# Kernel tuning notes

Hardware: AMD Instinct MI355X
Metric: run time of the kernel (lower is better)

## Reference

```python
import jax, jax.numpy as jnp
import numpy as np

B, N, D = 2, 2048, 1024          # batch, seq (= wh*ww), model dim
H, HD = 16, 64                   # heads, head_dim (inner_dim = H*HD = D)
MLP = 4096                       # SwiGLU hidden dim
WSY, WSX = 16, 32                # ws_y = wh//2, ws_x = ww//2  (wh=32, ww=64)
EPS = float(jnp.finfo(jnp.float32).eps)  # torch RMSNorm default eps


def setup_inputs() -> dict:
    key = jax.random.key(0)
    ks = jax.random.split(key, 8)
    return {
        "x": jax.random.normal(ks[0], (B, N, D), jnp.float32),
        "t": jax.random.normal(ks[1], (B,), jnp.float32),
        "dt": jax.random.normal(ks[2], (B, D), jnp.float32),
        "w_qkv": (jax.random.normal(ks[3], (3 * H * HD, D), jnp.float32) * 0.02),
        "w_o": (jax.random.normal(ks[4], (D, H * HD), jnp.float32) * 0.02),
        "w1": (jax.random.normal(ks[5], (2 * MLP, D), jnp.float32) * 0.02),
        "w2": (jax.random.normal(ks[6], (D, MLP), jnp.float32) * 0.02),
        "g_attn": jnp.ones((D,), jnp.float32),  # RMSNorm weight (attn)
        "g_ff": jnp.ones((D,), jnp.float32),    # RMSNorm weight (ffn)
    }


def _rms(x, g):
    return x * jax.lax.rsqrt(jnp.mean(x * x, axis=-1, keepdims=True) + EPS) * g


def _win(x):
    # 'b h (wc_y wc_x ws_y ws_x) d' -> 'b h (wc_y ws_y wc_x ws_x) d'
    b, h, n, d = x.shape
    return x.reshape(b, h, 2, 2, WSY, WSX, d).transpose(0, 1, 2, 4, 3, 5, 6).reshape(b, h, n, d)


def _unwin(x):
    # inverse of _win
    b, h, n, d = x.shape
    return x.reshape(b, h, 2, WSY, 2, WSX, d).transpose(0, 1, 2, 4, 3, 5, 6).reshape(b, h, n, d)


def reference(x, t, dt, w_qkv, w_o, w1, w2, g_attn, g_ff):
    # ---- SPAttention (pre-norm); all-to-all is identity on 1 device ----
    h = _rms(x, g_attn)
    qkv = h @ w_qkv.T                              # [B,N,3*H*HD]
    q, k, v = jnp.split(qkv, 3, axis=-1)
    as_heads = lambda z: z.reshape(B, N, H, HD).transpose(0, 2, 1, 3)  # b h n d
    q, k, v = _win(as_heads(q)), _win(as_heads(k)), _win(as_heads(v))
    # NOTE: the source computes RoPE2D(q), RoPE2D(k) but discards the result;
    # attention consumes the UNROTATED seq_gathered_q/k/v. Faithful: no rotation.
    scale = 1.0 / jnp.sqrt(jnp.float32(HD))        # SDPA default scale
    s = jnp.einsum('bhqd,bhkd->bhqk', q, k) * scale
    a = jax.nn.softmax(s, axis=-1)
    o = jnp.einsum('bhqk,bhkd->bhqd', a, v)
    o = _unwin(o).transpose(0, 2, 1, 3).reshape(B, N, H * HD)
    x = x + o @ w_o.T                               # residual
    # ---- SwiGLU FeedForward (pre-norm) + residual ----
    hf = _rms(x, g_ff)
    gate, up = jnp.split(hf @ w1.T, 2, axis=-1)
    return x + (jax.nn.silu(gate) * up) @ w2.T
```

## Files before the change

### kernel.cpp

```cpp
#include <hip/hip_runtime.h>
#include <cstdint>
#include <cstddef>

typedef __attribute__((ext_vector_type(8)))  __bf16 bf16x8;
typedef __attribute__((ext_vector_type(4)))  __bf16 bf16x4;
typedef __attribute__((ext_vector_type(4)))  float  f32x4;
typedef __attribute__((ext_vector_type(16))) float  f32x16;
typedef __attribute__((ext_vector_type(2)))  uint32_t u32x2;
typedef __attribute__((ext_vector_type(4)))  uint32_t u32x4;

#define MFMA_BF16(a, b, c) __builtin_amdgcn_mfma_f32_16x16x32_bf16((a), (b), (c), 0, 0, 0)
#define MFMA32(a, b, c)    __builtin_amdgcn_mfma_f32_32x32x16_bf16((a), (b), (c), 0, 0, 0)

__device__ __forceinline__ void gload_lds16(const __bf16* src, __bf16* lds_dst) {
    __builtin_amdgcn_global_load_lds(
        (const __attribute__((address_space(1))) void*)(const_cast<__bf16*>(src)),
        (__attribute__((address_space(3))) void*)(lds_dst), 16, 0, 0);
}

__device__ __forceinline__ uint32_t pack2(float a, float b) {
    uint16_t ua = __builtin_bit_cast(uint16_t, (__bf16)a);
    uint16_t ub = __builtin_bit_cast(uint16_t, (__bf16)b);
    return (uint32_t)ua | ((uint32_t)ub << 16);
}

__device__ __forceinline__ int xcd_swz(int lid, int n) {
    return (lid & 7) * (n >> 3) + (lid >> 3);
}

__global__ __launch_bounds__(256) void cvt4_kernel(const float* __restrict__ s0,
                                                   const float* __restrict__ s1,
                                                   const float* __restrict__ s2,
                                                   const float* __restrict__ s3,
                                                   __bf16* __restrict__ d0,
                                                   __bf16* __restrict__ d1,
                                                   __bf16* __restrict__ d2,
                                                   __bf16* __restrict__ d3) {
    int b = blockIdx.x;
    const float* s; __bf16* d; int off;
    if (b < 3072)       { s = s0; d = d0; off = b; }
    else if (b < 4096)  { s = s1; d = d1; off = b - 3072; }
    else if (b < 12288) { s = s2; d = d2; off = b - 4096; }
    else                { s = s3; d = d3; off = b - 12288; }
    int i = off * 256 + threadIdx.x;
    float4 v = reinterpret_cast<const float4*>(s)[i];
    bf16x4 o;
    o[0] = (__bf16)v.x; o[1] = (__bf16)v.y; o[2] = (__bf16)v.z; o[3] = (__bf16)v.w;
    reinterpret_cast<bf16x4*>(d)[i] = o;
}

__global__ __launch_bounds__(256) void rmsnorm_kernel(const float* __restrict__ x,
                                                      const float* __restrict__ g,
                                                      __bf16* __restrict__ out) {
    const int row = blockIdx.x;
    const int t = threadIdx.x;
    float4 v = reinterpret_cast<const float4*>(x + (size_t)row * 1024)[t];
    float ss = v.x * v.x + v.y * v.y + v.z * v.z + v.w * v.w;
#pragma unroll
    for (int m = 1; m < 64; m <<= 1) ss += __shfl_xor(ss, m);
    __shared__ float sred[4];
    if ((t & 63) == 0) sred[t >> 6] = ss;
    __syncthreads();
    float tot = sred[0] + sred[1] + sred[2] + sred[3];
    float rs = rsqrtf(tot * (1.0f / 1024.0f) + 1.1920928955078125e-07f);
    float4 gv = reinterpret_cast<const float4*>(g)[t];
    bf16x4 o;
    o[0] = (__bf16)(v.x * rs * gv.x);
    o[1] = (__bf16)(v.y * rs * gv.y);
    o[2] = (__bf16)(v.z * rs * gv.z);
    o[3] = (__bf16)(v.w * rs * gv.w);
    *reinterpret_cast<bf16x4*>(out + (size_t)row * 1024 + t * 4) = o;
}

__global__ __launch_bounds__(256) void rmsnorm_b_kernel(const __bf16* __restrict__ x,
                                                        const float* __restrict__ g,
                                                        __bf16* __restrict__ out) {
    const int row = blockIdx.x;
    const int t = threadIdx.x;
    bf16x4 v4 = reinterpret_cast<const bf16x4*>(x + (size_t)row * 1024)[t];
    float a = (float)v4[0], b = (float)v4[1], c = (float)v4[2], d = (float)v4[3];
    float ss = a * a + b * b + c * c + d * d;
#pragma unroll
    for (int m = 1; m < 64; m <<= 1) ss += __shfl_xor(ss, m);
    __shared__ float sred[4];
    if ((t & 63) == 0) sred[t >> 6] = ss;
    __syncthreads();
    float tot = sred[0] + sred[1] + sred[2] + sred[3];
    float rs = rsqrtf(tot * (1.0f / 1024.0f) + 1.1920928955078125e-07f);
    float4 gv = reinterpret_cast<const float4*>(g)[t];
    bf16x4 o;
    o[0] = (__bf16)(a * rs * gv.x);
    o[1] = (__bf16)(b * rs * gv.y);
    o[2] = (__bf16)(c * rs * gv.z);
    o[3] = (__bf16)(d * rs * gv.w);
    *reinterpret_cast<bf16x4*>(out + (size_t)row * 1024 + t * 4) = o;
}

template <int MODE, int NB>
__global__ __launch_bounds__(256) void gemm_nt(const __bf16* __restrict__ A, int lda,
                                               const __bf16* __restrict__ B, int ldb,
                                               __bf16* __restrict__ outb,
                                               float* __restrict__ outf,
                                               const float* __restrict__ resid,
                                               const __bf16* __restrict__ residb,
                                               int K, int ldo) {
    constexpr int BN = NB * 32;
    __shared__ __attribute__((aligned(16))) __bf16 As[128 * 64];
    __shared__ __attribute__((aligned(16))) __bf16 Bs[BN * 64];
    const int t = threadIdx.x;
    const int lane = t & 63;
    const int wid = t >> 6;
    const int nwg = gridDim.x * gridDim.y;
    const int sid = xcd_swz(blockIdx.x + blockIdx.y * gridDim.x, nwg);
    const int bm = sid % gridDim.x, bn = sid / gridDim.x;
    const int wm = (wid >> 1) * 64, wn = (wid & 1) * (NB * 16);
    f32x4 acc[4][NB] = {};

    for (int kt = 0; kt < K; kt += 64) {
        __syncthreads();
#pragma unroll
        for (int i = 0; i < 4; ++i) {
            int L = i * 256 + t;
            int r = L >> 3, s = L & 7;
            int c = s ^ (r & 7);
            gload_lds16(A + (size_t)(bm * 128 + r) * lda + kt + c * 8, As + L * 8);
        }
#pragma unroll
        for (int i = 0; i < NB; ++i) {
            int L = i * 256 + t;
            int r = L >> 3, s = L & 7;
            int c = s ^ (r & 7);
            int rb = bn * BN + r;
            int srow = (MODE == 2) ? ((rb >> 1) + ((rb & 1) << 12)) : rb;
            gload_lds16(B + (size_t)srow * ldb + kt + c * 8, Bs + L * 8);
        }
        __syncthreads();
#pragma unroll
        for (int ks = 0; ks < 2; ++ks) {
            bf16x8 af[4], bfr[NB];
#pragma unroll
            for (int mi = 0; mi < 4; ++mi) {
                int r = wm + mi * 16 + (lane & 15);
                int slot = (ks * 4 + (lane >> 4)) ^ (r & 7);
                af[mi] = *reinterpret_cast<const bf16x8*>(As + r * 64 + slot * 8);
            }
#pragma unroll
            for (int ni = 0; ni < NB; ++ni) {
                int r = wn + ni * 16 + (lane & 15);
                int slot = (ks * 4 + (lane >> 4)) ^ (r & 7);
                bfr[ni] = *reinterpret_cast<const bf16x8*>(Bs + r * 64 + slot * 8);
            }
            __builtin_amdgcn_s_setprio(1);
#pragma unroll
            for (int mi = 0; mi < 4; ++mi)
#pragma unroll
                for (int ni = 0; ni < NB; ++ni)
                    acc[mi][ni] = MFMA_BF16(af[mi], bfr[ni], acc[mi][ni]);
            __builtin_amdgcn_s_setprio(0);
        }
    }
    const int row0 = bm * 128 + wm + ((lane >> 4) << 2);
    const int col0 = bn * BN + wn + (lane & 15);
#pragma unroll
    for (int mi = 0; mi < 4; ++mi)
#pragma unroll
        for (int ni = 0; ni < NB; ++ni)
#pragma unroll
            for (int r2 = 0; r2 < 4; ++r2) {
                int row = row0 + mi * 16 + r2;
                int col = col0 + ni * 16;
                float v = acc[mi][ni][r2];
                size_t idx = (size_t)row * ldo + col;
                if (MODE == 0) {
                    outb[idx] = (__bf16)v;
                } else if (MODE == 1) {
                    outb[idx] = (__bf16)(v + resid[idx]);
                } else if (MODE == 3) {
                    outf[idx] = v + (float)residb[idx];
                } else {
                    float pv = __shfl_xor(v, 1);
                    if (!(lane & 1)) {
                        float sg = v / (1.0f + __expf(-v));
                        outb[(size_t)row * ldo + (col >> 1)] = (__bf16)(sg * pv);
                    }
                }
            }
}

__global__ __launch_bounds__(256) void vtrans_kernel(const __bf16* __restrict__ qkv,
                                                     __bf16* __restrict__ vt) {
    __shared__ __bf16 T[64][68];
    const int t = threadIdx.x;
    const int bh = blockIdx.y, b = bh >> 4, h = bh & 15;
    const int n0 = blockIdx.x * 64;
    const __bf16* vp = qkv + (size_t)b * 2048 * 3072 + 2048 + h * 64;
#pragma unroll
    for (int i = 0; i < 2; ++i) {
        int r = i * 32 + (t >> 3), c = t & 7;
        bf16x8 v = *reinterpret_cast<const bf16x8*>(vp + (size_t)(n0 + r) * 3072 + c * 8);
#pragma unroll
        for (int j = 0; j < 8; ++j) T[c * 8 + j][r] = v[j];
    }
    __syncthreads();
#pragma unroll
    for (int i = 0; i < 2; ++i) {
        int hd = i * 32 + (t >> 3), c = t & 7;
        bf16x8 v;
#pragma unroll
        for (int j = 0; j < 8; ++j) v[j] = T[hd][c * 8 + j];
        *reinterpret_cast<bf16x8*>(vt + ((size_t)bh * 64 + hd) * 2048 + n0 + c * 8) = v;
    }
}

__global__ __launch_bounds__(256) void attn_kernel(const __bf16* __restrict__ qkv,
                                                   const __bf16* __restrict__ vt,
                                                   __bf16* __restrict__ o) {
    __shared__ __attribute__((aligned(16))) __bf16 Ks[2][128 * 64];
    __shared__ __attribute__((aligned(16))) __bf16 Vs[2][64 * 128];
    const int t = threadIdx.x;
    const int lane = t & 63;
    const int w = t >> 6;
    const int hi = lane >> 5;
    const int l31 = lane & 31;
    const int nwg = gridDim.x * gridDim.y;
    const int sid = xcd_swz(blockIdx.x + blockIdx.y * gridDim.x, nwg);
    const int qb = sid % gridDim.x;
    const int bh = sid / gridDim.x;
    const int b = bh >> 4, h = bh & 15;
    const __bf16* qp = qkv + (size_t)b * 2048 * 3072 + h * 64;
    const __bf16* kp = qp + 1024;
    const __bf16* vtp = vt + (size_t)bh * 64 * 2048;
    const int q0 = qb * 128 + w * 32;

    const float SC = 0.18033688011112042f;
    bf16x8 qf[4];
#pragma unroll
    for (int s = 0; s < 4; ++s) {
        bf16x8 raw = *reinterpret_cast<const bf16x8*>(
            qp + (size_t)(q0 + l31) * 3072 + s * 16 + hi * 8);
        bf16x8 sc;
#pragma unroll
        for (int j = 0; j < 8; ++j) sc[j] = (__bf16)((float)raw[j] * SC);
        qf[s] = sc;
    }

    f32x16 oa[2] = {};
    float l_run = 0.0f;

    auto stage = [&](int buf, int kt) {
#pragma unroll
        for (int i = 0; i < 4; ++i) {
            int L = i * 256 + t;
            int r = L >> 3, s = L & 7;
            int c = s ^ (r & 7);
            gload_lds16(kp + (size_t)(kt + r) * 3072 + c * 8, &Ks[buf][L * 8]);
        }
#pragma unroll
        for (int i = 0; i < 4; ++i) {
            int L = i * 256 + t;
            int r = L >> 4, s = L & 15;
            int c = s ^ (r & 15);
            gload_lds16(vtp + (size_t)r * 2048 + kt + c * 8, &Vs[buf][L * 8]);
        }
    };
    stage(0, 0);
    __syncthreads();

    for (int kt = 0; kt < 2048; kt += 128) {
        const int buf = (kt >> 7) & 1;
        if (kt + 128 < 2048) stage(buf ^ 1, kt + 128);

#pragma unroll
        for (int h2 = 0; h2 < 2; ++h2) {
            f32x16 st[2];
#pragma unroll
            for (int r = 0; r < 16; ++r) { st[0][r] = -6.0f; st[1][r] = -6.0f; }
            __builtin_amdgcn_s_setprio(1);
#pragma unroll
            for (int s = 0; s < 4; ++s) {
#pragma unroll
                for (int mb = 0; mb < 2; ++mb) {
                    int r = h2 * 64 + mb * 32 + l31;
                    int sl = (s * 2 + hi) ^ (r & 7);
                    bf16x8 kf = *reinterpret_cast<const bf16x8*>(&Ks[buf][r * 64 + sl * 8]);
                    st[mb] = MFMA32(kf, qf[s], st[mb]);
                }
            }
            __builtin_amdgcn_s_setprio(0);

            float ps = 0.0f;
#pragma unroll
            for (int mb = 0; mb < 2; ++mb)
#pragma unroll
                for (int r = 0; r < 16; ++r) {
                    float p = exp2f(st[mb][r]);
                    st[mb][r] = p;
                    ps += p;
                }
            ps += __shfl_xor(ps, 32);
            l_run += ps;

            uint32_t pk[16];
#pragma unroll
            for (int mb = 0; mb < 2; ++mb)
#pragma unroll
                for (int i2 = 0; i2 < 8; ++i2)
                    pk[mb * 8 + i2] = pack2(st[mb][2 * i2], st[mb][2 * i2 + 1]);

            __builtin_amdgcn_s_setprio(1);
#pragma unroll
            for (int s2 = 0; s2 < 4; ++s2) {
                const int I0 = (s2 >> 1) * 8 + (s2 & 1) * 4;
                u32x2 w02 = __builtin_amdgcn_permlane32_swap(pk[I0], pk[I0 + 2], false, false);
                u32x2 w13 = __builtin_amdgcn_permlane32_swap(pk[I0 + 1], pk[I0 + 3], false, false);
                u32x4 fv;
                fv[0] = w02[0]; fv[1] = w13[0]; fv[2] = w02[1]; fv[3] = w13[1];
                bf16x8 pa = __builtin_bit_cast(bf16x8, fv);
#pragma unroll
                for (int nb = 0; nb < 2; ++nb) {
                    int rv = nb * 32 + l31;
                    int ch = h2 * 8 + s2 * 2 + hi;
                    int sl = ch ^ (rv & 15);
                    bf16x8 vf = *reinterpret_cast<const bf16x8*>(&Vs[buf][rv * 128 + sl * 8]);
                    oa[nb] = MFMA32(pa, vf, oa[nb]);
                }
            }
            __builtin_amdgcn_s_setprio(0);
        }
        __syncthreads();
    }

#pragma unroll
    for (int r = 0; r < 16; ++r) {
        int crow = (r & 3) + 8 * (r >> 2) + 4 * hi;
        float lv = __shfl(l_run, crow);
        float inv = 1.0f / lv;
        int row = q0 + crow;
        size_t base = ((size_t)b * 2048 + row) * 1024 + h * 64 + l31;
        o[base]      = (__bf16)(oa[0][r] * inv);
        o[base + 32] = (__bf16)(oa[1][r] * inv);
    }
}

extern "C" void kernel_launch(void* const* d_in, const int* in_sizes, int n_in,
                              void* d_out, int out_size, void* d_ws, size_t ws_size,
                              hipStream_t stream) {
    const float* x      = (const float*)d_in[0];
    const float* w_qkv  = (const float*)d_in[3];
    const float* w_o    = (const float*)d_in[4];
    const float* w1     = (const float*)d_in[5];
    const float* w2     = (const float*)d_in[6];
    const float* g_attn = (const float*)d_in[7];
    const float* g_ff   = (const float*)d_in[8];
    float* out = (float*)d_out;

    char* ws = (char*)d_ws;
    size_t off = 0;
    auto alloc = [&](size_t bytes) -> void* {
        void* p = ws + off;
        off += (bytes + 255) & ~(size_t)255;
        return p;
    };
    __bf16* wqkv_b = (__bf16*)alloc((size_t)3072 * 1024 * 2);
    __bf16* wo_b   = (__bf16*)alloc((size_t)1024 * 1024 * 2);
    __bf16* w1_b   = (__bf16*)alloc((size_t)8192 * 1024 * 2);
    __bf16* w2_b   = (__bf16*)alloc((size_t)1024 * 4096 * 2);
    __bf16* h_b    = (__bf16*)alloc((size_t)4096 * 1024 * 2);
    __bf16* qkv_b  = (__bf16*)alloc((size_t)4096 * 3072 * 2);
    __bf16* o_b    = (__bf16*)alloc((size_t)4096 * 1024 * 2);
    __bf16* x2b    = (__bf16*)alloc((size_t)4096 * 1024 * 2);
    __bf16* vt_b   = (__bf16*)alloc((size_t)32 * 64 * 2048 * 2);
    __bf16* act_b  = qkv_b;

    cvt4_kernel<<<16384, 256, 0, stream>>>(w_qkv, w_o, w1, w2,
                                           wqkv_b, wo_b, w1_b, w2_b);

    rmsnorm_kernel<<<4096, 256, 0, stream>>>(x, g_attn, h_b);
    gemm_nt<0, 4><<<dim3(32, 24), 256, 0, stream>>>(h_b, 1024, wqkv_b, 1024,
                                                    qkv_b, nullptr, nullptr, nullptr,
                                                    1024, 3072);
    vtrans_kernel<<<dim3(32, 32), 256, 0, stream>>>(qkv_b, vt_b);
    attn_kernel<<<dim3(16, 32), 256, 0, stream>>>(qkv_b, vt_b, o_b);
    gemm_nt<1, 2><<<dim3(32, 16), 256, 0, stream>>>(o_b, 1024, wo_b, 1024,
                                                    x2b, nullptr, x, nullptr,
                                                    1024, 1024);
    rmsnorm_b_kernel<<<4096, 256, 0, stream>>>(x2b, g_ff, h_b);
    gemm_nt<2, 4><<<dim3(32, 64), 256, 0, stream>>>(h_b, 1024, w1_b, 1024,
                                                    act_b, nullptr, nullptr, nullptr,
                                                    1024, 4096);
    gemm_nt<3, 4><<<dim3(32, 8), 256, 0, stream>>>(act_b, 4096, w2_b, 4096,
                                                   nullptr, out, nullptr, x2b,
                                                   4096, 1024);
}
```

Baseline: 317.0 us.

## Split-K attention, fuse V transpose into QKV GEMM, retile FFN GEMMs

The QKV GEMM epilogue now writes the V part directly in transposed layout, which removes the separate transpose kernel. Attention is split into two key halves along a grid z dimension. Each half writes unnormalized fp32 partial outputs and row sums, and a new combine kernel merges them. The attention loop also drops LDS double buffering in favor of load-then-barrier. The w1 GEMM gets a square-ish block-swizzle mapping, and the w2 GEMM uses NB=2 with twice as many blocks. These changes add parallelism and remove a kernel, but they add fp32 partial traffic and lose the load/compute overlap in attention.

```diff
diff --git a/kernel.cpp b/kernel.cpp
--- a/kernel.cpp
+++ b/kernel.cpp
@@ -96,13 +96,14 @@
     *reinterpret_cast<bf16x4*>(out + (size_t)row * 1024 + t * 4) = o;
 }
 
-template <int MODE, int NB>
+template <int MODE, int NB, int SQ>
 __global__ __launch_bounds__(256) void gemm_nt(const __bf16* __restrict__ A, int lda,
                                                const __bf16* __restrict__ B, int ldb,
                                                __bf16* __restrict__ outb,
                                                float* __restrict__ outf,
                                                const float* __restrict__ resid,
                                                const __bf16* __restrict__ residb,
+                                               __bf16* __restrict__ vt,
                                                int K, int ldo) {
     constexpr int BN = NB * 32;
     __shared__ __attribute__((aligned(16))) __bf16 As[128 * 64];
@@ -110,9 +111,17 @@
     const int t = threadIdx.x;
     const int lane = t & 63;
     const int wid = t >> 6;
-    const int nwg = gridDim.x * gridDim.y;
-    const int sid = xcd_swz(blockIdx.x + blockIdx.y * gridDim.x, nwg);
-    const int bm = sid % gridDim.x, bn = sid / gridDim.x;
+    int bm, bn;
+    if (SQ) {
+        int lid = blockIdx.x + blockIdx.y * gridDim.x;
+        int c = lid & 7, i = lid >> 3;
+        bm = (c & 1) * 16 + (i & 15);
+        bn = (c >> 1) * 16 + (i >> 4);
+    } else {
+        int nwg = gridDim.x * gridDim.y;
+        int sid = xcd_swz(blockIdx.x + blockIdx.y * gridDim.x, nwg);
+        bm = sid % gridDim.x; bn = sid / gridDim.x;
+    }
     const int wm = (wid >> 1) * 64, wn = (wid & 1) * (NB * 16);
     f32x4 acc[4][NB] = {};
 
@@ -161,6 +170,22 @@
     }
     const int row0 = bm * 128 + wm + ((lane >> 4) << 2);
     const int col0 = bn * BN + wn + (lane & 15);
+    if (MODE == 4 && bn >= 16) {
+#pragma unroll
+        for (int mi = 0; mi < 4; ++mi)
+#pragma unroll
+            for (int ni = 0; ni < NB; ++ni) {
+                bf16x4 o4;
+#pragma unroll
+                for (int r2 = 0; r2 < 4; ++r2) o4[r2] = (__bf16)acc[mi][ni][r2];
+                int n0 = row0 + mi * 16;
+                int bb = n0 >> 11, nn = n0 & 2047;
+                int vc = col0 + ni * 16 - 2048;
+                *reinterpret_cast<bf16x4*>(
+                    vt + ((size_t)(bb * 16 + (vc >> 6)) * 64 + (vc & 63)) * 2048 + nn) = o4;
+            }
+        return;
+    }
 #pragma unroll
     for (int mi = 0; mi < 4; ++mi)
 #pragma unroll
@@ -171,7 +196,7 @@
                 int col = col0 + ni * 16;
                 float v = acc[mi][ni][r2];
                 size_t idx = (size_t)row * ldo + col;
-                if (MODE == 0) {
+                if (MODE == 0 || MODE == 4) {
                     outb[idx] = (__bf16)v;
                 } else if (MODE == 1) {
                     outb[idx] = (__bf16)(v + resid[idx]);
@@ -187,36 +212,12 @@
             }
 }
 
-__global__ __launch_bounds__(256) void vtrans_kernel(const __bf16* __restrict__ qkv,
-                                                     __bf16* __restrict__ vt) {
-    __shared__ __bf16 T[64][68];
-    const int t = threadIdx.x;
-    const int bh = blockIdx.y, b = bh >> 4, h = bh & 15;
-    const int n0 = blockIdx.x * 64;
-    const __bf16* vp = qkv + (size_t)b * 2048 * 3072 + 2048 + h * 64;
-#pragma unroll
-    for (int i = 0; i < 2; ++i) {
-        int r = i * 32 + (t >> 3), c = t & 7;
-        bf16x8 v = *reinterpret_cast<const bf16x8*>(vp + (size_t)(n0 + r) * 3072 + c * 8);
-#pragma unroll
-        for (int j = 0; j < 8; ++j) T[c * 8 + j][r] = v[j];
-    }
-    __syncthreads();
-#pragma unroll
-    for (int i = 0; i < 2; ++i) {
-        int hd = i * 32 + (t >> 3), c = t & 7;
-        bf16x8 v;
-#pragma unroll
-        for (int j = 0; j < 8; ++j) v[j] = T[hd][c * 8 + j];
-        *reinterpret_cast<bf16x8*>(vt + ((size_t)bh * 64 + hd) * 2048 + n0 + c * 8) = v;
-    }
-}
-
 __global__ __launch_bounds__(256) void attn_kernel(const __bf16* __restrict__ qkv,
                                                    const __bf16* __restrict__ vt,
-                                                   __bf16* __restrict__ o) {
-    __shared__ __attribute__((aligned(16))) __bf16 Ks[2][128 * 64];
-    __shared__ __attribute__((aligned(16))) __bf16 Vs[2][64 * 128];
+                                                   float* __restrict__ opart,
+                                                   float* __restrict__ lpart) {
+    __shared__ __attribute__((aligned(16))) __bf16 Ks[128 * 64];
+    __shared__ __attribute__((aligned(16))) __bf16 Vs[64 * 128];
     const int t = threadIdx.x;
     const int lane = t & 63;
     const int w = t >> 6;
@@ -226,6 +227,7 @@
     const int sid = xcd_swz(blockIdx.x + blockIdx.y * gridDim.x, nwg);
     const int qb = sid % gridDim.x;
     const int bh = sid / gridDim.x;
+    const int kz = blockIdx.z;
     const int b = bh >> 4, h = bh & 15;
     const __bf16* qp = qkv + (size_t)b * 2048 * 3072 + h * 64;
     const __bf16* kp = qp + 1024;
@@ -247,28 +249,27 @@
     f32x16 oa[2] = {};
     float l_run = 0.0f;
 
-    auto stage = [&](int buf, int kt) {
+    auto stage = [&](int kt) {
 #pragma unroll
         for (int i = 0; i < 4; ++i) {
             int L = i * 256 + t;
             int r = L >> 3, s = L & 7;
             int c = s ^ (r & 7);
-            gload_lds16(kp + (size_t)(kt + r) * 3072 + c * 8, &Ks[buf][L * 8]);
+            gload_lds16(kp + (size_t)(kt + r) * 3072 + c * 8, &Ks[L * 8]);
         }
 #pragma unroll
         for (int i = 0; i < 4; ++i) {
             int L = i * 256 + t;
             int r = L >> 4, s = L & 15;
             int c = s ^ (r & 15);
-            gload_lds16(vtp + (size_t)r * 2048 + kt + c * 8, &Vs[buf][L * 8]);
+            gload_lds16(vtp + (size_t)r * 2048 + kt + c * 8, &Vs[L * 8]);
         }
     };
-    stage(0, 0);
-    __syncthreads();
-
-    for (int kt = 0; kt < 2048; kt += 128) {
-        const int buf = (kt >> 7) & 1;
-        if (kt + 128 < 2048) stage(buf ^ 1, kt + 128);
+
+    const int kt0 = kz * 1024;
+    for (int kt = kt0; kt < kt0 + 1024; kt += 128) {
+        stage(kt);
+        asm volatile("s_waitcnt vmcnt(0)\n\ts_barrier" ::: "memory");
 
 #pragma unroll
         for (int h2 = 0; h2 < 2; ++h2) {
@@ -282,7 +283,7 @@
                 for (int mb = 0; mb < 2; ++mb) {
                     int r = h2 * 64 + mb * 32 + l31;
                     int sl = (s * 2 + hi) ^ (r & 7);
-                    bf16x8 kf = *reinterpret_cast<const bf16x8*>(&Ks[buf][r * 64 + sl * 8]);
+                    bf16x8 kf = *reinterpret_cast<const bf16x8*>(&Ks[r * 64 + sl * 8]);
                     st[mb] = MFMA32(kf, qf[s], st[mb]);
                 }
             }
@@ -321,7 +322,7 @@
                     int rv = nb * 32 + l31;
                     int ch = h2 * 8 + s2 * 2 + hi;
                     int sl = ch ^ (rv & 15);
-                    bf16x8 vf = *reinterpret_cast<const bf16x8*>(&Vs[buf][rv * 128 + sl * 8]);
+                    bf16x8 vf = *reinterpret_cast<const bf16x8*>(&Vs[rv * 128 + sl * 8]);
                     oa[nb] = MFMA32(pa, vf, oa[nb]);
                 }
             }
@@ -333,13 +334,34 @@
 #pragma unroll
     for (int r = 0; r < 16; ++r) {
         int crow = (r & 3) + 8 * (r >> 2) + 4 * hi;
-        float lv = __shfl(l_run, crow);
-        float inv = 1.0f / lv;
         int row = q0 + crow;
-        size_t base = ((size_t)b * 2048 + row) * 1024 + h * 64 + l31;
-        o[base]      = (__bf16)(oa[0][r] * inv);
-        o[base + 32] = (__bf16)(oa[1][r] * inv);
-    }
+        size_t base = (size_t)kz * 4194304 + ((size_t)b * 2048 + row) * 1024 + h * 64 + l31;
+        opart[base]      = oa[0][r];
+        opart[base + 32] = oa[1][r];
+    }
+    if (hi == 0)
+        lpart[kz * 65536 + bh * 2048 + q0 + l31] = l_run;
+}
+
+__global__ __launch_bounds__(256) void attn_comb(const float* __restrict__ op,
+                                                 const float* __restrict__ lp,
+                                                 __bf16* __restrict__ o) {
+    const int row = blockIdx.x;
+    const int t = threadIdx.x;
+    const int b = row >> 11, q = row & 2047;
+    const int c0 = t * 4;
+    const int h = c0 >> 6;
+    const int li = (b * 16 + h) * 2048 + q;
+    float l = lp[li] + lp[65536 + li];
+    float inv = 1.0f / l;
+    float4 p0 = *reinterpret_cast<const float4*>(op + (size_t)row * 1024 + c0);
+    float4 p1 = *reinterpret_cast<const float4*>(op + 4194304 + (size_t)row * 1024 + c0);
+    bf16x4 o4;
+    o4[0] = (__bf16)((p0.x + p1.x) * inv);
+    o4[1] = (__bf16)((p0.y + p1.y) * inv);
+    o4[2] = (__bf16)((p0.z + p1.z) * inv);
+    o4[3] = (__bf16)((p0.w + p1.w) * inv);
+    *reinterpret_cast<bf16x4*>(o + (size_t)row * 1024 + c0) = o4;
 }
 
 extern "C" void kernel_launch(void* const* d_in, const int* in_sizes, int n_in,
@@ -370,25 +392,27 @@
     __bf16* o_b    = (__bf16*)alloc((size_t)4096 * 1024 * 2);
     __bf16* x2b    = (__bf16*)alloc((size_t)4096 * 1024 * 2);
     __bf16* vt_b   = (__bf16*)alloc((size_t)32 * 64 * 2048 * 2);
+    float*  opart  = (float*)alloc((size_t)2 * 4096 * 1024 * 4);
+    float*  lpart  = (float*)alloc((size_t)2 * 32 * 2048 * 4);
     __bf16* act_b  = qkv_b;
 
     cvt4_kernel<<<16384, 256, 0, stream>>>(w_qkv, w_o, w1, w2,
                                            wqkv_b, wo_b, w1_b, w2_b);
 
     rmsnorm_kernel<<<4096, 256, 0, stream>>>(x, g_attn, h_b);
-    gemm_nt<0, 4><<<dim3(32, 24), 256, 0, stream>>>(h_b, 1024, wqkv_b, 1024,
-                                                    qkv_b, nullptr, nullptr, nullptr,
-                                                    1024, 3072);
-    vtrans_kernel<<<dim3(32, 32), 256, 0, stream>>>(qkv_b, vt_b);
-    attn_kernel<<<dim3(16, 32), 256, 0, stream>>>(qkv_b, vt_b, o_b);
-    gemm_nt<1, 2><<<dim3(32, 16), 256, 0, stream>>>(o_b, 1024, wo_b, 1024,
-                                                    x2b, nullptr, x, nullptr,
-                                                    1024, 1024);
+    gemm_nt<4, 4, 0><<<dim3(32, 24), 256, 0, stream>>>(h_b, 1024, wqkv_b, 1024,
+                                                       qkv_b, nullptr, nullptr, nullptr,
+                                                       vt_b, 1024, 3072);
+    attn_kernel<<<dim3(16, 32, 2), 256, 0, stream>>>(qkv_b, vt_b, opart, lpart);
+    attn_comb<<<4096, 256, 0, stream>>>(opart, lpart, o_b);
+    gemm_nt<1, 2, 0><<<dim3(32, 16), 256, 0, stream>>>(o_b, 1024, wo_b, 1024,
+                                                       x2b, nullptr, x, nullptr,
+                                                       nullptr, 1024, 1024);
     rmsnorm_b_kernel<<<4096, 256, 0, stream>>>(x2b, g_ff, h_b);
-    gemm_nt<2, 4><<<dim3(32, 64), 256, 0, stream>>>(h_b, 1024, w1_b, 1024,
-                                                    act_b, nullptr, nullptr, nullptr,
-                                                    1024, 4096);
-    gemm_nt<3, 4><<<dim3(32, 8), 256, 0, stream>>>(act_b, 4096, w2_b, 4096,
-                                                   nullptr, out, nullptr, x2b,
-                                                   4096, 1024);
-}
+    gemm_nt<2, 4, 1><<<dim3(32, 64), 256, 0, stream>>>(h_b, 1024, w1_b, 1024,
+                                                       act_b, nullptr, nullptr, nullptr,
+                                                       nullptr, 1024, 4096);
+    gemm_nt<3, 2, 0><<<dim3(32, 16), 256, 0, stream>>>(act_b, 4096, w2_b, 4096,
+                                                       nullptr, out, nullptr, x2b,
+                                                       nullptr, 4096, 1024);
+}
```

Result: faster. 308.6 us (-2.6%).
